# Kernel tuning notes

Measured on AMD Instinct MI355X. Metric: run time of the kernel, lower is better.

The kernel has to match this reference:

```python
import jax, jax.numpy as jnp
import numpy as np

H = 16          # num heads
HD = 88         # head dim = 1408 / 16
IMG = 336
PATCH = 14
THETA = 10000.0
IDX = IMG // PATCH          # 24 patches per side
SEQ = IDX * IDX + 1         # 576 patches + 1 CLS slot = 577


def _vision_rope_cos_sin():
    # Faithful to HF Llama4VisionRotaryEmbedding (rope_type='llama4', complex64):
    # 2D rope over (x, y) patch coordinates; CLS token gets zero rotation.
    img_idx = np.arange(IDX * IDX, dtype=np.int64).reshape(-1, 1)
    img_idx = np.concatenate([img_idx, img_idx[:1]], axis=0)
    img_idx[-1, -1] = -2  # CLS token marker
    fx = img_idx % IDX
    fy = img_idx // IDX
    freq_dim = HD // 2  # 44
    rope_freq = 1.0 / (THETA ** (np.arange(0, freq_dim, 2)[: freq_dim // 2].astype(np.float64) / freq_dim))
    freqs_x = np.repeat((fx + 1)[..., None] * rope_freq[None, None, :], 2, axis=-1)
    freqs_y = np.repeat((fy + 1)[..., None] * rope_freq[None, None, :], 2, axis=-1)
    freqs = np.concatenate([freqs_x, freqs_y], axis=-1)[..., ::2]  # [SEQ, 1, HD//2]
    freqs = np.where(img_idx.reshape(-1, 1, 1) < 0, 0.0, freqs)
    return jnp.asarray(np.cos(freqs), jnp.float32), jnp.asarray(np.sin(freqs), jnp.float32)


def _apply_rope(x, cos, sin):
    # x: [B, S, H, HD]; treat last dim as HD//2 complex pairs, rotate by e^{i*freq}
    xr = x.reshape(*x.shape[:-1], HD // 2, 2)
    a, b = xr[..., 0], xr[..., 1]               # [B, S, H, HD//2]
    out_r = a * cos - b * sin                   # cos/sin [S,1,HD//2] broadcast over B,H
    out_i = a * sin + b * cos
    return jnp.stack([out_r, out_i], axis=-1).reshape(x.shape)


def setup_inputs() -> dict:
    key = jax.random.key(0)
    ks = jax.random.split(key, 9)
    D = H * HD  # 1408
    B, S = 32, SEQ
    s = 0.02
    return {
        "hidden_states": jax.random.normal(ks[0], (B, S, D), jnp.float32),
        "wq": jax.random.normal(ks[1], (D, D), jnp.float32) * s,
        "bq": jax.random.normal(ks[2], (D,), jnp.float32) * s,
        "wk": jax.random.normal(ks[3], (D, D), jnp.float32) * s,
        "bk": jax.random.normal(ks[4], (D,), jnp.float32) * s,
        "wv": jax.random.normal(ks[5], (D, D), jnp.float32) * s,
        "bv": jax.random.normal(ks[6], (D,), jnp.float32) * s,
        "wo": jax.random.normal(ks[7], (D, D), jnp.float32) * s,
        "bo": jax.random.normal(ks[8], (D,), jnp.float32) * s,
    }


def reference(hidden_states, wq, bq, wk, bk, wv, bv, wo, bo):
    B, S, D = hidden_states.shape
    cos, sin = _vision_rope_cos_sin()
    # QKV projections (torch Linear convention: y = x @ W.T + b)
    q = (hidden_states @ wq.T + bq).reshape(B, S, H, HD)
    k = (hidden_states @ wk.T + bk).reshape(B, S, H, HD)
    v = (hidden_states @ wv.T + bv).reshape(B, S, H, HD)
    q = _apply_rope(q, cos, sin)
    k = _apply_rope(k, cos, sin)
    # Full (non-causal) self-attention
    scores = jnp.einsum('bqhd,bkhd->bhqk', q, k) * (HD ** -0.5)
    probs = jax.nn.softmax(scores, axis=-1)
    attn = jnp.einsum('bhqk,bkhd->bqhd', probs, v).reshape(B, S, D)
    return attn @ wo.T + bo
```

## Files before the change

kernel.cpp:

```cpp
#include <hip/hip_runtime.h>
#include <hip/hip_bf16.h>
#include <cstdint>
#include <cstddef>

#define NHEADS 16
#define HDIM   88
#define SEQLEN 577
#define NBATCH 32
#define DMODEL 1408
#define MROWS  (NBATCH * SEQLEN)
#define MTILES 145
#define MPAD   (MTILES * 128)
#define SP     592
#define DP     96
#define NFREQ  44
#define NBH    (NBATCH * NHEADS)
#define PADELEMS 6056

typedef __attribute__((ext_vector_type(8))) short short8;
typedef __attribute__((ext_vector_type(4))) short short4v;
typedef __attribute__((ext_vector_type(4))) float floatx4;

__device__ __forceinline__ unsigned short f2bf(float f) {
    union { float f; unsigned u; } v; v.f = f;
    unsigned u = v.u;
    u += 0x7fffu + ((u >> 16) & 1u);
    return (unsigned short)(u >> 16);
}

__device__ __forceinline__ void gload_lds16(const void* g, void* lds) {
    __builtin_amdgcn_global_load_lds(
        (__attribute__((address_space(1))) unsigned int*)(void*)(g ? (void*)g : (void*)g),
        (__attribute__((address_space(3))) unsigned int*)lds, 16, 0, 0);
}

__global__ void l4v_rope_table(float* __restrict__ cos_t, float* __restrict__ sin_t) {
    int idx = blockIdx.x * blockDim.x + threadIdx.x;
    if (idx >= SEQLEN * NFREQ) return;
    int s = idx / NFREQ, j = idx % NFREQ;
    float ang = 0.0f;
    if (s != SEQLEN - 1) {
        int coord = (j < 22) ? (s % 24) : (s / 24);
        int i = (j < 22) ? j : j - 22;
        float rf = __expf(-(2.0f * (float)i / 44.0f) * 9.21034037197618f);
        ang = (float)(coord + 1) * rf;
    }
    cos_t[idx] = cosf(ang);
    sin_t[idx] = sinf(ang);
}

__global__ void l4v_cvt_bf16(const float* __restrict__ in, unsigned short* __restrict__ out, int n) {
    int i = (blockIdx.x * blockDim.x + threadIdx.x) * 4;
    if (i + 3 < n) {
        float4 f = *(const float4*)(in + i);
        ushort4 o;
        o.x = f2bf(f.x); o.y = f2bf(f.y); o.z = f2bf(f.z); o.w = f2bf(f.w);
        *(ushort4*)(out + i) = o;
    } else {
        for (; i < n; i++) out[i] = f2bf(in[i]);
    }
}

__global__ void l4v_padzero(unsigned short* __restrict__ qb,
                            unsigned short* __restrict__ kb,
                            unsigned short* __restrict__ vb) {
    int idx = blockIdx.x * blockDim.x + threadIdx.x;
    if (idx >= NBH * PADELEMS) return;
    int bh = idx / PADELEMS, r = idx % PADELEMS;
    size_t off;
    if (r < 15 * 96) {
        int row = SEQLEN + r / 96, col = r % 96;
        off = ((size_t)bh * SP + row) * DP + col;
    } else {
        int rr = r - 15 * 96;
        int row = rr / 8, col = 88 + (rr % 8);
        off = ((size_t)bh * SP + row) * DP + col;
    }
    qb[off] = 0; kb[off] = 0; vb[off] = 0;
}

__global__ __launch_bounds__(256, 2)
void l4v_gemm128(const unsigned short* __restrict__ A,
                 const unsigned short* __restrict__ Bw,
                 const float* __restrict__ bias,
                 const float* __restrict__ cos_t,
                 const float* __restrict__ sin_t,
                 unsigned short* __restrict__ out_bf,
                 float* __restrict__ out_f32,
                 int mode)
{
    __shared__ __align__(16) unsigned short a_sm[128 * 32];
    __shared__ __align__(16) unsigned short b_sm[128 * 32];

    const int tid  = threadIdx.x;
    const int lane = tid & 63;
    const int w    = tid >> 6;
    const int quad = lane >> 4;
    const int c    = lane & 15;
    const int wr   = w >> 1;
    const int wc   = w & 1;
    const int m0   = blockIdx.y * 128;
    const int n0   = blockIdx.x * 128;

    floatx4 acc[4][4];
#pragma unroll
    for (int i = 0; i < 4; i++)
#pragma unroll
        for (int j = 0; j < 4; j++) acc[i][j] = (floatx4)0.0f;

    const int chunk0 = w * 128 + lane;
    const int chunk1 = w * 128 + 64 + lane;
    const int r0 = chunk0 >> 2, ch0 = chunk0 & 3;
    const int r1 = chunk1 >> 2, ch1 = chunk1 & 3;
    const unsigned short* Ab = A  + (size_t)m0 * DMODEL;
    const unsigned short* Bb = Bw + (size_t)n0 * DMODEL;

    for (int k0 = 0; k0 < DMODEL; k0 += 32) {
        gload_lds16(Ab + (size_t)r0 * DMODEL + k0 + ch0 * 8, a_sm + (w * 128) * 8);
        gload_lds16(Ab + (size_t)r1 * DMODEL + k0 + ch1 * 8, a_sm + (w * 128 + 64) * 8);
        gload_lds16(Bb + (size_t)r0 * DMODEL + k0 + ch0 * 8, b_sm + (w * 128) * 8);
        gload_lds16(Bb + (size_t)r1 * DMODEL + k0 + ch1 * 8, b_sm + (w * 128 + 64) * 8);
        __syncthreads();
        short8 af[4], bfr[4];
#pragma unroll
        for (int mt = 0; mt < 4; mt++)
            af[mt] = *(const short8*)(a_sm + (wr * 64 + mt * 16 + c) * 32 + quad * 8);
#pragma unroll
        for (int nt = 0; nt < 4; nt++)
            bfr[nt] = *(const short8*)(b_sm + (wc * 64 + nt * 16 + c) * 32 + quad * 8);
#pragma unroll
        for (int mt = 0; mt < 4; mt++)
#pragma unroll
            for (int nt = 0; nt < 4; nt++)
                acc[mt][nt] = __builtin_amdgcn_mfma_f32_16x16x32_bf16(af[mt], bfr[nt], acc[mt][nt], 0, 0, 0);
        __syncthreads();
    }

    if (mode == 3) {
#pragma unroll
        for (int mt = 0; mt < 4; mt++) {
            int mbase = m0 + wr * 64 + mt * 16 + quad * 4;
#pragma unroll
            for (int nt = 0; nt < 4; nt++) {
                int n = n0 + wc * 64 + nt * 16 + c;
                float bi = bias[n];
#pragma unroll
                for (int r = 0; r < 4; r++) {
                    int m = mbase + r;
                    if (m < MROWS) out_f32[(size_t)m * DMODEL + n] = acc[mt][nt][r] + bi;
                }
            }
        }
        return;
    }

    const bool rope = (mode < 2);
#pragma unroll
    for (int mt = 0; mt < 4; mt++) {
        int mbase = m0 + wr * 64 + mt * 16 + quad * 4;
#pragma unroll
        for (int nt = 0; nt < 4; nt++) {
            int n = n0 + wc * 64 + nt * 16 + c;
            float bi = bias[n];
            int h = n / HDIM, d = n % HDIM, j = d >> 1;
#pragma unroll
            for (int r = 0; r < 4; r++) {
                int m = mbase + r;
                int s = m % SEQLEN;
                int b = m / SEQLEN;
                float v = acc[mt][nt][r] + bi;
                float outv = v;
                if (rope) {
                    float pv = __shfl_xor(v, 1);
                    float cs = cos_t[s * NFREQ + j];
                    float sn = sin_t[s * NFREQ + j];
                    outv = ((d & 1) == 0) ? (v * cs - pv * sn) : (pv * sn + v * cs);
                }
                if (m < MROWS)
                    out_bf[((size_t)(b * NHEADS + h) * SP + s) * DP + d] = f2bf(outv);
            }
        }
    }
}

__global__ __launch_bounds__(256, 2)
void l4v_attn(const unsigned short* __restrict__ Q,
              const unsigned short* __restrict__ K,
              const unsigned short* __restrict__ V,
              unsigned short* __restrict__ Obuf)
{
    __shared__ __align__(16) unsigned short k_sm[64 * DP];
    __shared__ __align__(16) unsigned short v_sm[64 * DP];
    __shared__ __align__(16) unsigned short v_tr[96 * 68];
    __shared__ __align__(16) unsigned short p_sm[4][16 * 68];

    const int tid  = threadIdx.x;
    const int lane = tid & 63;
    const int w    = tid >> 6;
    const int quad = lane >> 4;
    const int c    = lane & 15;
    const int qt   = blockIdx.x;
    const int bh   = blockIdx.y;
    const size_t base = (size_t)bh * SP * DP;

    short8 aq[3];
    {
        int qrow = qt * 64 + w * 16 + c;
        if (qrow > SP - 1) qrow = SP - 1;
#pragma unroll
        for (int ks = 0; ks < 3; ks++)
            aq[ks] = *(const short8*)(Q + base + (size_t)qrow * DP + ks * 32 + quad * 8);
    }

    float m_run[4], l_run[4];
    floatx4 o_acc[6];
#pragma unroll
    for (int r = 0; r < 4; r++) { m_run[r] = -INFINITY; l_run[r] = 0.0f; }
#pragma unroll
    for (int i = 0; i < 6; i++) o_acc[i] = (floatx4)0.0f;

    const float sl2e = 0.10660035817780522f * 1.4426950408889634f;

    for (int kt = 0; kt < 10; kt++) {
#pragma unroll
        for (int i = 0; i < 3; i++) {
            int chnk = w * 192 + i * 64 + lane;
            int row = chnk / 12, ch = chnk % 12;
            int krow = kt * 64 + row;
            if (krow > SP - 1) krow = SP - 1;
            gload_lds16(K + base + (size_t)krow * DP + ch * 8, k_sm + (w * 192 + i * 64) * 8);
            gload_lds16(V + base + (size_t)krow * DP + ch * 8, v_sm + (w * 192 + i * 64) * 8);
        }
        __syncthreads();

        floatx4 sc[4];
#pragma unroll
        for (int nt = 0; nt < 4; nt++) {
            sc[nt] = (floatx4)0.0f;
#pragma unroll
            for (int ks = 0; ks < 3; ks++) {
                short8 bk = *(const short8*)(k_sm + (nt * 16 + c) * DP + ks * 32 + quad * 8);
                sc[nt] = __builtin_amdgcn_mfma_f32_16x16x32_bf16(aq[ks], bk, sc[nt], 0, 0, 0);
            }
        }

#pragma unroll
        for (int i = 0; i < 3; i++) {
            int chnk = w * 192 + i * 64 + lane;
            int srow = chnk / 12, ch = chnk % 12;
            short8 vv = *(const short8*)(v_sm + srow * DP + ch * 8);
#pragma unroll
            for (int jj = 0; jj < 8; jj++) {
                int d = ch * 8 + jj;
                v_tr[d * 68 + (((srow >> 2) ^ (d & 15)) << 2) + (srow & 3)] =
                    (unsigned short)vv[jj];
            }
        }

        float t[4][4];
#pragma unroll
        for (int nt = 0; nt < 4; nt++) {
            int skcol = kt * 64 + nt * 16 + c;
            bool valid = (skcol < SEQLEN);
#pragma unroll
            for (int r = 0; r < 4; r++)
                t[nt][r] = valid ? sc[nt][r] * sl2e : -INFINITY;
        }

        float mnew[4], alpha[4];
#pragma unroll
        for (int r = 0; r < 4; r++) {
            float v = fmaxf(fmaxf(t[0][r], t[1][r]), fmaxf(t[2][r], t[3][r]));
#pragma unroll
            for (int off = 1; off < 16; off <<= 1) v = fmaxf(v, __shfl_xor(v, off));
            mnew[r] = fmaxf(m_run[r], v);
            alpha[r] = exp2f(m_run[r] - mnew[r]);
            m_run[r] = mnew[r];
        }

        float p[4][4];
#pragma unroll
        for (int nt = 0; nt < 4; nt++)
#pragma unroll
            for (int r = 0; r < 4; r++)
                p[nt][r] = exp2f(t[nt][r] - mnew[r]);

#pragma unroll
        for (int r = 0; r < 4; r++) {
            float sm = p[0][r] + p[1][r] + p[2][r] + p[3][r];
#pragma unroll
            for (int off = 1; off < 16; off <<= 1) sm += __shfl_xor(sm, off);
            l_run[r] = l_run[r] * alpha[r] + sm;
        }

#pragma unroll
        for (int nt = 0; nt < 4; nt++)
#pragma unroll
            for (int r = 0; r < 4; r++)
                p_sm[w][(quad * 4 + r) * 68 + nt * 16 + c] = f2bf(p[nt][r]);

#pragma unroll
        for (int i = 0; i < 6; i++)
#pragma unroll
            for (int r = 0; r < 4; r++)
                o_acc[i][r] *= alpha[r];

        __syncthreads();

#pragma unroll
        for (int kp = 0; kp < 2; kp++) {
            short8 ap;
            {
                short4v lo = *(const short4v*)(&p_sm[w][c * 68 + kp * 32 + quad * 8]);
                short4v hi = *(const short4v*)(&p_sm[w][c * 68 + kp * 32 + quad * 8 + 4]);
#pragma unroll
                for (int t4 = 0; t4 < 4; t4++) { ap[t4] = lo[t4]; ap[t4 + 4] = hi[t4]; }
            }
#pragma unroll
            for (int d2 = 0; d2 < 6; d2++) {
                int drow = d2 * 16 + c;
                int c4 = kp * 8 + quad * 2;
                short4v lo = *(const short4v*)(v_tr + drow * 68 + (((c4 + 0) ^ c) << 2));
                short4v hi = *(const short4v*)(v_tr + drow * 68 + (((c4 + 1) ^ c) << 2));
                short8 bv;
#pragma unroll
                for (int t4 = 0; t4 < 4; t4++) { bv[t4] = lo[t4]; bv[t4 + 4] = hi[t4]; }
                o_acc[d2] = __builtin_amdgcn_mfma_f32_16x16x32_bf16(ap, bv, o_acc[d2], 0, 0, 0);
            }
        }
    }

    const int b = bh >> 4, h = bh & 15;
#pragma unroll
    for (int r = 0; r < 4; r++) {
        int sq = qt * 64 + w * 16 + quad * 4 + r;
        float il = 1.0f / l_run[r];
        if (sq < SEQLEN) {
            size_t rowoff = ((size_t)b * SEQLEN + sq) * DMODEL + h * HDIM;
#pragma unroll
            for (int d2 = 0; d2 < 6; d2++) {
                int d = d2 * 16 + c;
                if (d < HDIM) Obuf[rowoff + d] = f2bf(o_acc[d2][r] * il);
            }
        }
    }
}

extern "C" void kernel_launch(void* const* d_in, const int* in_sizes, int n_in,
                              void* d_out, int out_size, void* d_ws, size_t ws_size,
                              hipStream_t stream)
{
    const float* hs = (const float*)d_in[0];
    const float* wq = (const float*)d_in[1];
    const float* bq = (const float*)d_in[2];
    const float* wk = (const float*)d_in[3];
    const float* bk = (const float*)d_in[4];
    const float* wv = (const float*)d_in[5];
    const float* bv = (const float*)d_in[6];
    const float* wo = (const float*)d_in[7];
    const float* bo = (const float*)d_in[8];
    float* out = (float*)d_out;

    char* ws = (char*)d_ws;
    size_t off = 0;
    auto alloc = [&](size_t bytes) -> char* {
        char* p = ws + off;
        off += (bytes + 255) & ~(size_t)255;
        return p;
    };

    unsigned short* hs_bf = (unsigned short*)alloc((size_t)MPAD * DMODEL * 2);
    unsigned short* wq_bf = (unsigned short*)alloc((size_t)DMODEL * DMODEL * 2);
    unsigned short* wk_bf = (unsigned short*)alloc((size_t)DMODEL * DMODEL * 2);
    unsigned short* wv_bf = (unsigned short*)alloc((size_t)DMODEL * DMODEL * 2);
    unsigned short* wo_bf = (unsigned short*)alloc((size_t)DMODEL * DMODEL * 2);
    unsigned short* qb    = (unsigned short*)alloc((size_t)NBH * SP * DP * 2);
    unsigned short* kb    = (unsigned short*)alloc((size_t)NBH * SP * DP * 2);
    unsigned short* vbuf  = (unsigned short*)alloc((size_t)NBH * SP * DP * 2);
    float* cos_t = (float*)alloc((size_t)SEQLEN * NFREQ * 4);
    float* sin_t = (float*)alloc((size_t)SEQLEN * NFREQ * 4);
    unsigned short* attn_bf = hs_bf;

    if (off > ws_size) return;

    l4v_rope_table<<<dim3((SEQLEN * NFREQ + 255) / 256), dim3(256), 0, stream>>>(cos_t, sin_t);
    l4v_padzero<<<dim3((NBH * PADELEMS + 255) / 256), dim3(256), 0, stream>>>(qb, kb, vbuf);

    const int nhs = MROWS * DMODEL;
    l4v_cvt_bf16<<<dim3(nhs / 4 / 256), dim3(256), 0, stream>>>(hs, hs_bf, nhs);
    const int nw = DMODEL * DMODEL;
    l4v_cvt_bf16<<<dim3(nw / 4 / 256), dim3(256), 0, stream>>>(wq, wq_bf, nw);
    l4v_cvt_bf16<<<dim3(nw / 4 / 256), dim3(256), 0, stream>>>(wk, wk_bf, nw);
    l4v_cvt_bf16<<<dim3(nw / 4 / 256), dim3(256), 0, stream>>>(wv, wv_bf, nw);
    l4v_cvt_bf16<<<dim3(nw / 4 / 256), dim3(256), 0, stream>>>(wo, wo_bf, nw);

    dim3 ggrid(DMODEL / 128, MTILES);
    l4v_gemm128<<<ggrid, dim3(256), 0, stream>>>(hs_bf, wq_bf, bq, cos_t, sin_t, qb, nullptr, 0);
    l4v_gemm128<<<ggrid, dim3(256), 0, stream>>>(hs_bf, wk_bf, bk, cos_t, sin_t, kb, nullptr, 1);
    l4v_gemm128<<<ggrid, dim3(256), 0, stream>>>(hs_bf, wv_bf, bv, cos_t, sin_t, vbuf, nullptr, 2);

    l4v_attn<<<dim3(10, NBH), dim3(256), 0, stream>>>(qb, kb, vbuf, attn_bf);

    l4v_gemm128<<<ggrid, dim3(256), 0, stream>>>(attn_bf, wo_bf, bo, cos_t, sin_t, nullptr, out, 3);
}
```

Measured before the change: 1.207 ms.

## Drop LDS V transpose; read swizzled V columns directly and pad K rows

The explicit transpose of the V tile into a separate shared buffer is removed. V is now loaded into shared memory with an XOR chunk swizzle, and the PV MFMA operand is gathered directly as eight 16-bit column reads. The K tile row stride is padded to 104 to reduce bank conflicts. One mid-loop barrier is replaced by a single end-of-iteration barrier. This removes the transpose work and shared-memory footprint, but adds many scalar LDS reads per MFMA operand.

```diff
diff --git a/kernel.cpp b/kernel.cpp
--- a/kernel.cpp
+++ b/kernel.cpp
@@ -189,9 +189,8 @@
               const unsigned short* __restrict__ V,
               unsigned short* __restrict__ Obuf)
 {
-    __shared__ __align__(16) unsigned short k_sm[64 * DP];
-    __shared__ __align__(16) unsigned short v_sm[64 * DP];
-    __shared__ __align__(16) unsigned short v_tr[96 * 68];
+    __shared__ __align__(16) unsigned short k_sm[64 * 104];
+    __shared__ __align__(16) unsigned short v_sm[64 * 96];
     __shared__ __align__(16) unsigned short p_sm[4][16 * 68];
 
     const int tid  = threadIdx.x;
@@ -223,13 +222,24 @@
 
     for (int kt = 0; kt < 10; kt++) {
 #pragma unroll
+        for (int i = 0; i < 4; i++) {
+            int chnk = i * 256 + tid;
+            if (chnk < 64 * 13) {
+                int row = chnk / 13, pos = chnk - row * 13;
+                int gpos = (pos < 12) ? pos : 0;
+                int krow = kt * 64 + row;
+                if (krow > SP - 1) krow = SP - 1;
+                gload_lds16(K + base + (size_t)krow * DP + gpos * 8, k_sm + chnk * 8);
+            }
+        }
+#pragma unroll
         for (int i = 0; i < 3; i++) {
-            int chnk = w * 192 + i * 64 + lane;
-            int row = chnk / 12, ch = chnk % 12;
+            int chnk = i * 256 + tid;
+            int row = chnk / 12, pos = chnk - row * 12;
+            int gpos = pos ^ ((row >> 3) & 3);
             int krow = kt * 64 + row;
             if (krow > SP - 1) krow = SP - 1;
-            gload_lds16(K + base + (size_t)krow * DP + ch * 8, k_sm + (w * 192 + i * 64) * 8);
-            gload_lds16(V + base + (size_t)krow * DP + ch * 8, v_sm + (w * 192 + i * 64) * 8);
+            gload_lds16(V + base + (size_t)krow * DP + gpos * 8, v_sm + chnk * 8);
         }
         __syncthreads();
 
@@ -239,21 +249,8 @@
             sc[nt] = (floatx4)0.0f;
 #pragma unroll
             for (int ks = 0; ks < 3; ks++) {
-                short8 bk = *(const short8*)(k_sm + (nt * 16 + c) * DP + ks * 32 + quad * 8);
+                short8 bk = *(const short8*)(k_sm + (nt * 16 + c) * 104 + ks * 32 + quad * 8);
                 sc[nt] = __builtin_amdgcn_mfma_f32_16x16x32_bf16(aq[ks], bk, sc[nt], 0, 0, 0);
-            }
-        }
-
-#pragma unroll
-        for (int i = 0; i < 3; i++) {
-            int chnk = w * 192 + i * 64 + lane;
-            int srow = chnk / 12, ch = chnk % 12;
-            short8 vv = *(const short8*)(v_sm + srow * DP + ch * 8);
-#pragma unroll
-            for (int jj = 0; jj < 8; jj++) {
-                int d = ch * 8 + jj;
-                v_tr[d * 68 + (((srow >> 2) ^ (d & 15)) << 2) + (srow & 3)] =
-                    (unsigned short)vv[jj];
             }
         }
 
@@ -304,8 +301,6 @@
 #pragma unroll
             for (int r = 0; r < 4; r++)
                 o_acc[i][r] *= alpha[r];
-
-        __syncthreads();
 
 #pragma unroll
         for (int kp = 0; kp < 2; kp++) {
@@ -318,16 +313,15 @@
             }
 #pragma unroll
             for (int d2 = 0; d2 < 6; d2++) {
-                int drow = d2 * 16 + c;
-                int c4 = kp * 8 + quad * 2;
-                short4v lo = *(const short4v*)(v_tr + drow * 68 + (((c4 + 0) ^ c) << 2));
-                short4v hi = *(const short4v*)(v_tr + drow * 68 + (((c4 + 1) ^ c) << 2));
+                int posx = (((d2 * 2 + (c >> 3)) ^ quad) << 3) + (c & 7);
                 short8 bv;
 #pragma unroll
-                for (int t4 = 0; t4 < 4; t4++) { bv[t4] = lo[t4]; bv[t4 + 4] = hi[t4]; }
+                for (int j = 0; j < 8; j++)
+                    bv[j] = (short)v_sm[(kp * 32 + quad * 8 + j) * 96 + posx];
                 o_acc[d2] = __builtin_amdgcn_mfma_f32_16x16x32_bf16(ap, bv, o_acc[d2], 0, 0, 0);
             }
         }
+        __syncthreads();
     }
 
     const int b = bh >> 4, h = bh & 15;
```

New measurement: 1.033 ms. 14.5% less time.
